# Performance work log

Hardware: AMD Instinct MI355X
Metric: run time of the kernel (lower is better)

The kernel has to match this reference:

```python
import jax, jax.numpy as jnp
import numpy as np

NEG_INF = -1e5  # module default neg_inf


def setup_inputs() -> dict:
    key = jax.random.key(0)
    k1, k2 = jax.random.split(key)
    B, T, V, U = 64, 1000, 512, 256
    log_posteriors = jax.random.normal(k1, (B, T, V), dtype=jnp.float32)
    lens = jnp.ones((B,), dtype=jnp.float32)
    phns = jax.random.randint(k2, (B, U), 0, V)
    phn_lens = jnp.ones((B,), dtype=jnp.float32)
    return {"log_posteriors": log_posteriors, "lens": lens, "phns": phns, "phn_lens": phn_lens}


def _forward_scores(log_posteriors, lens, phns, phn_lens):
    B, T, V = log_posteriors.shape
    U = phns.shape[1]
    lens_abs = jnp.round(lens * T).astype(jnp.int32)
    phn_lens_abs = jnp.round(phn_lens * U).astype(jnp.int32)

    # --- pi: all initial mass on first phoneme ---
    pi = jnp.full((B, U), NEG_INF, dtype=jnp.float32).at[:, 0].set(0.0)

    # --- transition log-probs: self-loop + advance-by-one, length-masked, row log_softmax ---
    base = jnp.eye(U, dtype=jnp.float32) + jnp.eye(U, k=1, dtype=jnp.float32)  # (U,U)
    m = jnp.arange(U)[None, :] < phn_lens_abs[:, None]  # (B,U) valid-phoneme mask
    m2 = m[:, :, None] & m[:, None, :]  # (B,U,U)
    masked = base[None, :, :] * m2.astype(jnp.float32)
    logits = jnp.where(masked == 1.0, 1.0, -jnp.inf)
    trans = jax.nn.log_softmax(logits, axis=2)
    # nan (all -inf rows) and -inf -> neg_inf, as in the torch module
    trans = jnp.where(jnp.isnan(trans) | jnp.isinf(trans), NEG_INF, trans)  # (B,U,U)

    # --- emissions rearranged to phoneme-sequence order: (B, U, T) as (T, B, U) scan seq ---
    mask_t = jnp.arange(T)[None, :] < lens_abs[:, None]  # (B,T)
    ep = jnp.where(mask_t[:, :, None], log_posteriors, NEG_INF)
    idx = jnp.broadcast_to(phns[:, None, :], (B, T, U))
    gathered = jnp.take_along_axis(ep, idx, axis=2)  # (B,T,U)
    emiss = jnp.where(m[:, None, :], gathered, NEG_INF)  # (B,T,U)
    emiss_seq = jnp.swapaxes(emiss, 0, 1)  # (T,B,U)

    # --- forward DP: alpha[t,i] = logsumexp_j(trans[j,i] + alpha[t-1,j]) + emiss[t,i] ---
    transT = jnp.swapaxes(trans, 1, 2)  # (B, to, from)
    alpha0 = pi + emiss_seq[0]  # (B,U), unmasked as in torch (masked entries ~2*neg_inf anyway)

    def step(alpha, e_t):
        x = jax.nn.logsumexp(transT + alpha[:, None, :], axis=2)  # batch_log_matvecmul
        alpha_new = jnp.where(m, x + e_t, NEG_INF)
        return alpha_new, None

    alphaT, _ = jax.lax.scan(step, alpha0, emiss_seq[1:])
    return jax.nn.logsumexp(alphaT, axis=1)  # (B,) log-likelihoods


def reference(log_posteriors, lens, phns, phn_lens):
    return _forward_scores(log_posteriors, lens, phns, phn_lens)
```

## Files before the change

kernel.cpp:

```cpp
#include <hip/hip_runtime.h>
#include <math.h>

constexpr int Bc = 64;
constexpr int Tc = 1000;
constexpr int Vc = 512;
constexpr int Uc = 256;
constexpr int CH = 50;
constexpr int NCH = Tc / CH;
constexpr int PW = 7;
constexpr int SLOTS = 4;

constexpr int GW = 4;
constexpr int GSL = 5;
constexpr int GROWS = GW * GSL * 2;
constexpr int GBLK = Tc / GROWS;

#define NEG_INF_F (-100000.0f)
#define LOG2E_F 1.44269504088896340736f
#define LN2_F 0.69314718055994530942f
#define DEAD_F (-1.0e9f)

__device__ __forceinline__ float fexp2(float x) {
#if __has_builtin(__builtin_amdgcn_exp2f)
    return __builtin_amdgcn_exp2f(x);
#else
    return __expf(x * LN2_F);
#endif
}
__device__ __forceinline__ float flog2(float x) {
#if __has_builtin(__builtin_amdgcn_logf)
    return __builtin_amdgcn_logf(x);
#else
    return __logf(x) * LOG2E_F;
#endif
}

__device__ __forceinline__ float l2add(float x, float y) {
    float m = fmaxf(x, y);
    float p = fexp2(-fabsf(x - y));
    return m + flog2(1.0f + p);
}

__device__ __forceinline__ float waveshr1(float x, float lane0val) {
    return __int_as_float(__builtin_amdgcn_update_dpp(
        __float_as_int(lane0val), __float_as_int(x),
        0x138 , 0xF, 0xF, false));
}

__device__ __forceinline__ void hmm_step(float rr[4], const float4 ev) {
    float nb0 = waveshr1(rr[3], DEAD_F);
    float e[4] = {ev.x, ev.y, ev.z, ev.w};
    float nb[4] = {nb0, rr[0], rr[1], rr[2]};
#pragma unroll
    for (int c = 0; c < 4; ++c) {
        float x = rr[c], y = nb[c];
        float m = fmaxf(x, y);
        float p = fexp2(-fabsf(x - y));
        float me = m + e[c];
        rr[c] = me + flog2(1.0f + p);
    }
}

__device__ __forceinline__ void dma16(const float* gsrc, float* lds, int lane) {
    typedef const __attribute__((address_space(1))) unsigned int* gp_t;
    typedef __attribute__((address_space(3))) unsigned int* lp_t;
    __builtin_amdgcn_global_load_lds((gp_t)(const void*)(gsrc + 4 * lane),
                                     (lp_t)(void*)lds, 16, 0, 0);
}

__global__ __launch_bounds__(256, 4) void gather_kernel(
    const float* __restrict__ lp, const float* __restrict__ lens,
    const int* __restrict__ phns, const float* __restrict__ phn_lens,
    float* __restrict__ e2) {
    __shared__ float stage[GW][GSL][Vc];
    const int b = blockIdx.x;
    const int t0 = blockIdx.y * GROWS;
    const int tid = threadIdx.x;
    const int wave = tid >> 6;
    const int lane = tid & 63;
    const int Tv = (int)rintf(lens[b] * (float)Tc);
    const int Uv = (int)rintf(phn_lens[b] * (float)Uc);
    const float* lpb = lp + (size_t)b * Tc * Vc;
    float* e2b = e2 + ((size_t)b * Tc + t0) * Uc;

    int col[4];
    float off[4];
    bool pv[4];
    int4 cc = *(const int4*)(phns + (size_t)b * Uc + 4 * lane);
    int c4[4] = {cc.x, cc.y, cc.z, cc.w};
#pragma unroll
    for (int c = 0; c < 4; ++c) {
        int v = c4[c];
        v = v < 0 ? 0 : (v > Vc - 1 ? Vc - 1 : v);
        col[c] = v;
        int i = 4 * lane + c;
        pv[c] = (i < Uv);
        off[c] = (i == Uv - 1) ? 0.0f : -1.0f;
    }

    float* stw = &stage[wave][0][0];
#pragma unroll
    for (int half = 0; half < 2; ++half) {
#pragma unroll
        for (int j = 0; j < GSL; ++j) {
            int r = wave + (half * GSL + j) * GW;
            const float* gsrc = lpb + (size_t)(t0 + r) * Vc;
            float* st = stw + j * Vc;
            dma16(gsrc, st, lane);
            dma16(gsrc + 256, st + 256, lane);
        }
        __builtin_amdgcn_s_waitcnt(0x0f70);
#pragma unroll
        for (int j = 0; j < GSL; ++j) {
            int r = wave + (half * GSL + j) * GW;
            const bool tv = (t0 + r) < Tv;
            const float* st = stw + j * Vc;
            float ev[4];
#pragma unroll
            for (int c = 0; c < 4; ++c) {
                float e = st[col[c]];
                ev[c] = (pv[c] && tv) ? fmaf(e, LOG2E_F, off[c])
                                      : (NEG_INF_F * LOG2E_F + off[c]);
            }
            *(float4*)(e2b + (size_t)r * Uc + 4 * lane) =
                make_float4(ev[0], ev[1], ev[2], ev[3]);
        }
    }
}

__global__ __launch_bounds__(128, 1) void scan_kernel(
    const float* __restrict__ e2, const float* __restrict__ phn_lens,
    float* __restrict__ out) {
    __shared__ float ebuf[2][CH][Uc];
    const int b = blockIdx.x;
    const int tid = threadIdx.x;
    const int wave = tid >> 6;
    const int lane = tid & 63;
    const int Uv = (int)rintf(phn_lens[b] * (float)Uc);
    const float* eb = e2 + (size_t)b * Tc * Uc;
    float rr[4];

    auto fill = [&](int k) {
        const float* src = eb + (size_t)k * CH * Uc;
        float* dst = &ebuf[k & 1][0][0];
#pragma unroll 5
        for (int r = 0; r < CH; ++r)
            dma16(src + (size_t)r * Uc, dst + r * Uc, lane);
    };

    auto consume = [&](int k) {
        const float4* base = (const float4*)&ebuf[k & 1][0][0] + lane;
        int r = 0;
        if (k == 0) {
            float4 e0 = base[0];
            float ea[4] = {e0.x, e0.y, e0.z, e0.w};
#pragma unroll
            for (int c = 0; c < 4; ++c)
                rr[c] = ((4 * lane + c == 0) ? 0.0f : DEAD_F) + ea[c];
            r = 1;
        }
        float4 q0, q1, q2, q3;
        if (r + 0 < CH) q0 = base[(r + 0) * 64];
        if (r + 1 < CH) q1 = base[(r + 1) * 64];
        if (r + 2 < CH) q2 = base[(r + 2) * 64];
        if (r + 3 < CH) q3 = base[(r + 3) * 64];
        while (r + 4 <= CH) {
            float4 e0 = q0, e1 = q1, e2v = q2, e3 = q3;
            if (r + 4 < CH) q0 = base[(r + 4) * 64];
            if (r + 5 < CH) q1 = base[(r + 5) * 64];
            if (r + 6 < CH) q2 = base[(r + 6) * 64];
            if (r + 7 < CH) q3 = base[(r + 7) * 64];
            hmm_step(rr, e0);
            hmm_step(rr, e1);
            hmm_step(rr, e2v);
            hmm_step(rr, e3);
            r += 4;
        }
        if (r + 0 < CH) hmm_step(rr, q0);
        if (r + 1 < CH) hmm_step(rr, q1);
        if (r + 2 < CH) hmm_step(rr, q2);
    };

    if (wave == 1) fill(0);
    __syncthreads();
    for (int k = 0; k < NCH; ++k) {
        if (wave == 1) {
            if (k + 1 < NCH) fill(k + 1);
        } else {
            consume(k);
        }
        __syncthreads();
    }

    if (wave == 0) {
        float a[4];
#pragma unroll
        for (int c = 0; c < 4; ++c)
            a[c] = rr[c] + ((4 * lane + c == Uv - 1) ? 0.0f : 1.0f);
        float r2 = l2add(l2add(a[0], a[1]), l2add(a[2], a[3]));
#pragma unroll
        for (int o = 32; o >= 1; o >>= 1) {
            float t = __shfl_xor(r2, o, 64);
            r2 = l2add(r2, t);
        }
        if (lane == 0) out[b] = r2 * LN2_F;
    }
}

__global__ __launch_bounds__(512, 1) void fused_hmm_kernel(
    const float* __restrict__ lp, const float* __restrict__ lens,
    const int* __restrict__ phns, const float* __restrict__ phn_lens,
    float* __restrict__ out) {
    __shared__ float ebuf[2][CH][Uc];
    __shared__ float stage[PW][SLOTS][Vc];
    const int b = blockIdx.x;
    const int tid = threadIdx.x;
    const int wave = tid >> 6;
    const int lane = tid & 63;
    const int Tv = (int)rintf(lens[b] * (float)Tc);
    const int Uv = (int)rintf(phn_lens[b] * (float)Uc);
    const float* lpb = lp + (size_t)b * Tc * Vc;

    int col[4];
    float off[4];
    bool pv[4];
    float rr[4];

    if (wave > 0) {
        int4 cc = *(const int4*)(phns + (size_t)b * Uc + 4 * lane);
        int c4[4] = {cc.x, cc.y, cc.z, cc.w};
#pragma unroll
        for (int c = 0; c < 4; ++c) {
            int v = c4[c];
            v = v < 0 ? 0 : (v > Vc - 1 ? Vc - 1 : v);
            col[c] = v;
            int i = 4 * lane + c;
            pv[c] = (i < Uv);
            off[c] = (i == Uv - 1) ? 0.0f : -1.0f;
        }
    }

    auto fill = [&](int k) {
        float* dst = &ebuf[k & 1][0][0];
        const int tb = k * CH;
        const int r0 = wave - 1;
        float* stw = &stage[wave - 1][0][0];
#pragma unroll
        for (int half = 0; half < 2; ++half) {
#pragma unroll
            for (int jj = 0; jj < SLOTS; ++jj) {
                int r = r0 + (half * SLOTS + jj) * PW;
                if (r < CH) {
                    const float* gsrc = lpb + (size_t)(tb + r) * Vc;
                    float* st = stw + jj * Vc;
                    dma16(gsrc, st, lane);
                    dma16(gsrc + 256, st + 256, lane);
                }
            }
            __builtin_amdgcn_s_waitcnt(0x0f70);
#pragma unroll
            for (int jj = 0; jj < SLOTS; ++jj) {
                int r = r0 + (half * SLOTS + jj) * PW;
                if (r < CH) {
                    const bool tv = (tb + r) < Tv;
                    const float* st = stw + jj * Vc;
                    float ev[4];
#pragma unroll
                    for (int c = 0; c < 4; ++c) {
                        float e = st[col[c]];
                        ev[c] = (pv[c] && tv) ? fmaf(e, LOG2E_F, off[c])
                                              : (NEG_INF_F * LOG2E_F + off[c]);
                    }
                    *(float4*)(dst + r * Uc + 4 * lane) =
                        make_float4(ev[0], ev[1], ev[2], ev[3]);
                }
            }
        }
    };

    auto consume = [&](int k) {
        const float4* base = (const float4*)&ebuf[k & 1][0][0] + lane;
        int r = 0;
        if (k == 0) {
            float4 e0 = base[0];
            float ea[4] = {e0.x, e0.y, e0.z, e0.w};
#pragma unroll
            for (int c = 0; c < 4; ++c)
                rr[c] = ((4 * lane + c == 0) ? 0.0f : DEAD_F) + ea[c];
            r = 1;
        }
        float4 q0, q1, q2, q3;
        if (r + 0 < CH) q0 = base[(r + 0) * 64];
        if (r + 1 < CH) q1 = base[(r + 1) * 64];
        if (r + 2 < CH) q2 = base[(r + 2) * 64];
        if (r + 3 < CH) q3 = base[(r + 3) * 64];
        while (r + 4 <= CH) {
            float4 e0 = q0, e1 = q1, e2 = q2, e3 = q3;
            if (r + 4 < CH) q0 = base[(r + 4) * 64];
            if (r + 5 < CH) q1 = base[(r + 5) * 64];
            if (r + 6 < CH) q2 = base[(r + 6) * 64];
            if (r + 7 < CH) q3 = base[(r + 7) * 64];
            hmm_step(rr, e0);
            hmm_step(rr, e1);
            hmm_step(rr, e2);
            hmm_step(rr, e3);
            r += 4;
        }
        if (r + 0 < CH) hmm_step(rr, q0);
        if (r + 1 < CH) hmm_step(rr, q1);
        if (r + 2 < CH) hmm_step(rr, q2);
    };

    if (wave > 0) fill(0);
    __syncthreads();
    for (int k = 0; k < NCH; ++k) {
        if (wave > 0) {
            if (k + 1 < NCH) fill(k + 1);
        } else {
            consume(k);
        }
        __syncthreads();
    }

    if (wave == 0) {
        float a[4];
#pragma unroll
        for (int c = 0; c < 4; ++c)
            a[c] = rr[c] + ((4 * lane + c == Uv - 1) ? 0.0f : 1.0f);
        float r2 = l2add(l2add(a[0], a[1]), l2add(a[2], a[3]));
#pragma unroll
        for (int o = 32; o >= 1; o >>= 1) {
            float t = __shfl_xor(r2, o, 64);
            r2 = l2add(r2, t);
        }
        if (lane == 0) out[b] = r2 * LN2_F;
    }
}

extern "C" void kernel_launch(void* const* d_in, const int* in_sizes, int n_in,
                              void* d_out, int out_size, void* d_ws, size_t ws_size,
                              hipStream_t stream) {
    const float* lp = (const float*)d_in[0];
    const float* lens = (const float*)d_in[1];
    const int* phns = (const int*)d_in[2];
    const float* phn_lens = (const float*)d_in[3];
    float* out = (float*)d_out;
    (void)in_sizes; (void)n_in; (void)out_size;

    const size_t need = (size_t)Bc * Tc * Uc * sizeof(float);
    if (d_ws != nullptr && ws_size >= need) {
        float* e2 = (float*)d_ws;
        gather_kernel<<<dim3(Bc, GBLK), 256, 0, stream>>>(lp, lens, phns,
                                                          phn_lens, e2);
        scan_kernel<<<Bc, 128, 0, stream>>>(e2, phn_lens, out);
    } else {
        fused_hmm_kernel<<<Bc, 512, 0, stream>>>(lp, lens, phns, phn_lens, out);
    }
}
```

Before: 289.7 us.

## Run HMM forward recursion in linear domain with f64 and per-chunk rescaling

The gather kernel now writes exp2 of the scaled emissions, so the scan works in linear probability space. Each step becomes an add plus a multiply in double precision instead of max/exp2/log2 in log space. To keep values from underflowing, the state vector is rescaled by a power of two after every chunk and the exponent is accumulated. The scan also drops to a single wave that issues its own async LDS fills, and the gather block shape changes. The risks are heavier f64 throughput and the precision limits of the linear domain.

```diff
diff --git a/kernel.cpp b/kernel.cpp
--- a/kernel.cpp
+++ b/kernel.cpp
@@ -10,9 +10,9 @@
 constexpr int PW = 7;
 constexpr int SLOTS = 4;
 
-constexpr int GW = 4;
-constexpr int GSL = 5;
-constexpr int GROWS = GW * GSL * 2;
+constexpr int GW = 2;
+constexpr int GNR = 10;
+constexpr int GROWS = GW * GNR;
 constexpr int GBLK = Tc / GROWS;
 
 #define NEG_INF_F (-100000.0f)
@@ -47,6 +47,25 @@
         0x138 , 0xF, 0xF, false));
 }
 
+__device__ __forceinline__ double waveshr1_f64(double x) {
+    int lo = __double2loint(x), hi = __double2hiint(x);
+    int slo = __builtin_amdgcn_update_dpp(0, lo, 0x138, 0xF, 0xF, false);
+    int shi = __builtin_amdgcn_update_dpp(0, hi, 0x138, 0xF, 0xF, false);
+    return __hiloint2double(shi, slo);
+}
+
+__device__ __forceinline__ void hmm_step_f64(double rr[4], const float4 ev) {
+    double nb0 = waveshr1_f64(rr[3]);
+    double s0 = rr[0] + nb0;
+    double s1 = rr[1] + rr[0];
+    double s2 = rr[2] + rr[1];
+    double s3 = rr[3] + rr[2];
+    rr[0] = s0 * (double)ev.x;
+    rr[1] = s1 * (double)ev.y;
+    rr[2] = s2 * (double)ev.z;
+    rr[3] = s3 * (double)ev.w;
+}
+
 __device__ __forceinline__ void hmm_step(float rr[4], const float4 ev) {
     float nb0 = waveshr1(rr[3], DEAD_F);
     float e[4] = {ev.x, ev.y, ev.z, ev.w};
@@ -68,11 +87,11 @@
                                      (lp_t)(void*)lds, 16, 0, 0);
 }
 
-__global__ __launch_bounds__(256, 4) void gather_kernel(
+__global__ __launch_bounds__(128, 2) void gather_kernel(
     const float* __restrict__ lp, const float* __restrict__ lens,
     const int* __restrict__ phns, const float* __restrict__ phn_lens,
-    float* __restrict__ e2) {
-    __shared__ float stage[GW][GSL][Vc];
+    float* __restrict__ el) {
+    __shared__ float stage[GW][GNR][Vc];
     const int b = blockIdx.x;
     const int t0 = blockIdx.y * GROWS;
     const int tid = threadIdx.x;
@@ -81,7 +100,7 @@
     const int Tv = (int)rintf(lens[b] * (float)Tc);
     const int Uv = (int)rintf(phn_lens[b] * (float)Uc);
     const float* lpb = lp + (size_t)b * Tc * Vc;
-    float* e2b = e2 + ((size_t)b * Tc + t0) * Uc;
+    float* elb = el + ((size_t)b * Tc + t0) * Uc;
 
     int col[4];
     float off[4];
@@ -100,45 +119,47 @@
 
     float* stw = &stage[wave][0][0];
 #pragma unroll
-    for (int half = 0; half < 2; ++half) {
-#pragma unroll
-        for (int j = 0; j < GSL; ++j) {
-            int r = wave + (half * GSL + j) * GW;
-            const float* gsrc = lpb + (size_t)(t0 + r) * Vc;
-            float* st = stw + j * Vc;
-            dma16(gsrc, st, lane);
-            dma16(gsrc + 256, st + 256, lane);
-        }
-        __builtin_amdgcn_s_waitcnt(0x0f70);
-#pragma unroll
-        for (int j = 0; j < GSL; ++j) {
-            int r = wave + (half * GSL + j) * GW;
+    for (int j = 0; j < GNR; ++j) {
+        int r = wave + j * GW;
+        const float* gsrc = lpb + (size_t)(t0 + r) * Vc;
+        float* st = stw + j * Vc;
+        dma16(gsrc, st, lane);
+        dma16(gsrc + 256, st + 256, lane);
+    }
+
+    auto do_rows = [&](int j0) {
+#pragma unroll
+        for (int j = j0; j < j0 + GNR / 2; ++j) {
+            int r = wave + j * GW;
             const bool tv = (t0 + r) < Tv;
             const float* st = stw + j * Vc;
             float ev[4];
 #pragma unroll
             for (int c = 0; c < 4; ++c) {
                 float e = st[col[c]];
-                ev[c] = (pv[c] && tv) ? fmaf(e, LOG2E_F, off[c])
-                                      : (NEG_INF_F * LOG2E_F + off[c]);
+                ev[c] = (pv[c] && tv) ? fexp2(fmaf(e, LOG2E_F, off[c])) : 0.0f;
             }
-            *(float4*)(e2b + (size_t)r * Uc + 4 * lane) =
+            *(float4*)(elb + (size_t)r * Uc + 4 * lane) =
                 make_float4(ev[0], ev[1], ev[2], ev[3]);
         }
-    }
-}
-
-__global__ __launch_bounds__(128, 1) void scan_kernel(
-    const float* __restrict__ e2, const float* __restrict__ phn_lens,
+    };
+
+    __builtin_amdgcn_s_waitcnt(0x0f7A);
+    do_rows(0);
+    __builtin_amdgcn_s_waitcnt(0x0f70);
+    do_rows(GNR / 2);
+}
+
+__global__ __launch_bounds__(64, 1) void scan_kernel(
+    const float* __restrict__ el, const float* __restrict__ phn_lens,
     float* __restrict__ out) {
     __shared__ float ebuf[2][CH][Uc];
     const int b = blockIdx.x;
-    const int tid = threadIdx.x;
-    const int wave = tid >> 6;
-    const int lane = tid & 63;
+    const int lane = threadIdx.x & 63;
     const int Uv = (int)rintf(phn_lens[b] * (float)Uc);
-    const float* eb = e2 + (size_t)b * Tc * Uc;
-    float rr[4];
+    const float* eb = el + (size_t)b * Tc * Uc;
+    double rr[4];
+    float S = 0.0f;
 
     auto fill = [&](int k) {
         const float* src = eb + (size_t)k * CH * Uc;
@@ -156,7 +177,7 @@
             float ea[4] = {e0.x, e0.y, e0.z, e0.w};
 #pragma unroll
             for (int c = 0; c < 4; ++c)
-                rr[c] = ((4 * lane + c == 0) ? 0.0f : DEAD_F) + ea[c];
+                rr[c] = (4 * lane + c == 0) ? (double)ea[c] : 0.0;
             r = 1;
         }
         float4 q0, q1, q2, q3;
@@ -170,41 +191,41 @@
             if (r + 5 < CH) q1 = base[(r + 5) * 64];
             if (r + 6 < CH) q2 = base[(r + 6) * 64];
             if (r + 7 < CH) q3 = base[(r + 7) * 64];
-            hmm_step(rr, e0);
-            hmm_step(rr, e1);
-            hmm_step(rr, e2v);
-            hmm_step(rr, e3);
+            hmm_step_f64(rr, e0);
+            hmm_step_f64(rr, e1);
+            hmm_step_f64(rr, e2v);
+            hmm_step_f64(rr, e3);
             r += 4;
         }
-        if (r + 0 < CH) hmm_step(rr, q0);
-        if (r + 1 < CH) hmm_step(rr, q1);
-        if (r + 2 < CH) hmm_step(rr, q2);
-    };
-
-    if (wave == 1) fill(0);
-    __syncthreads();
+        if (r + 0 < CH) hmm_step_f64(rr, q0);
+        if (r + 1 < CH) hmm_step_f64(rr, q1);
+        if (r + 2 < CH) hmm_step_f64(rr, q2);
+    };
+
+    fill(0);
+    __builtin_amdgcn_s_waitcnt(0x0f70);
     for (int k = 0; k < NCH; ++k) {
-        if (wave == 1) {
-            if (k + 1 < NCH) fill(k + 1);
-        } else {
-            consume(k);
-        }
-        __syncthreads();
-    }
-
-    if (wave == 0) {
-        float a[4];
-#pragma unroll
-        for (int c = 0; c < 4; ++c)
-            a[c] = rr[c] + ((4 * lane + c == Uv - 1) ? 0.0f : 1.0f);
-        float r2 = l2add(l2add(a[0], a[1]), l2add(a[2], a[3]));
-#pragma unroll
-        for (int o = 32; o >= 1; o >>= 1) {
-            float t = __shfl_xor(r2, o, 64);
-            r2 = l2add(r2, t);
-        }
-        if (lane == 0) out[b] = r2 * LN2_F;
-    }
+        if (k + 1 < NCH) fill(k + 1);
+        consume(k);
+        double m = fmax(fmax(rr[0], rr[1]), fmax(rr[2], rr[3]));
+#pragma unroll
+        for (int o = 32; o >= 1; o >>= 1) m = fmax(m, __shfl_xor(m, o, 64));
+        if (m > 0.0) {
+            int ik = ((__double2hiint(m) >> 20) & 0x7ff) - 1023;
+            S += (float)ik;
+            const double sc = __hiloint2double((1023 - ik) << 20, 0);
+            rr[0] *= sc; rr[1] *= sc; rr[2] *= sc; rr[3] *= sc;
+        }
+        __builtin_amdgcn_s_waitcnt(0x0f70);
+    }
+
+    double a = 0.0;
+#pragma unroll
+    for (int c = 0; c < 4; ++c)
+        a += rr[c] * ((4 * lane + c == Uv - 1) ? 1.0 : 2.0);
+#pragma unroll
+    for (int o = 32; o >= 1; o >>= 1) a += __shfl_xor(a, o, 64);
+    if (lane == 0) out[b] = (flog2((float)a) + S) * LN2_F;
 }
 
 __global__ __launch_bounds__(512, 1) void fused_hmm_kernel(
@@ -349,10 +370,10 @@
 
     const size_t need = (size_t)Bc * Tc * Uc * sizeof(float);
     if (d_ws != nullptr && ws_size >= need) {
-        float* e2 = (float*)d_ws;
-        gather_kernel<<<dim3(Bc, GBLK), 256, 0, stream>>>(lp, lens, phns,
-                                                          phn_lens, e2);
-        scan_kernel<<<Bc, 128, 0, stream>>>(e2, phn_lens, out);
+        float* el = (float*)d_ws;
+        gather_kernel<<<dim3(Bc, GBLK), 128, 0, stream>>>(lp, lens, phns,
+                                                          phn_lens, el);
+        scan_kernel<<<Bc, 64, 0, stream>>>(el, phn_lens, out);
     } else {
         fused_hmm_kernel<<<Bc, 512, 0, stream>>>(lp, lens, phns, phn_lens, out);
     }
```

Measured after the change: 280.6 us. 1.03x faster.
